# Performance work log

Hardware: AMD Instinct MI355X
Metric: run time of the kernel (lower is better)

The kernel has to match this reference:

```python
import jax, jax.numpy as jnp
import numpy as np

TAU = 2.0      # LIFNode default tau
V_TH = 1.0     # default v_threshold
ALPHA = 4.0    # surrogate.Sigmoid default alpha

@jax.custom_vjp
def spike_fn(x):
    # heaviside: spike if membrane potential crosses threshold
    return (x >= 0.0).astype(x.dtype)

def _spike_fwd(x):
    return spike_fn(x), x

def _spike_bwd(x, g):
    s = jax.nn.sigmoid(ALPHA * x)
    return (g * ALPHA * s * (1.0 - s),)

spike_fn.defvjp(_spike_fwd, _spike_bwd)

def lif_step(v, inp):
    # decay_input=True, v_reset=0.0 (hard reset):
    # v <- v + (inp - v)/tau ; spike = H(v - v_th) ; v <- v*(1-spike)
    v = v + (inp - v) / TAU
    s = spike_fn(v - V_TH)
    v = v * (1.0 - s)
    return v, s

def setup_inputs() -> dict:
    key = jax.random.key(0)
    k_x, k1, k2, k3 = jax.random.split(key, 4)
    T, B, H, W = 16, 64, 150, 400
    x = jax.random.normal(k_x, (T, B, H, W), dtype=jnp.float32)
    # torch Linear default init: U(-1/sqrt(fan_in), 1/sqrt(fan_in))
    def lin_init(k, out_f, in_f):
        bound = 1.0 / np.sqrt(in_f)
        return jax.random.uniform(k, (out_f, in_f), dtype=jnp.float32,
                                  minval=-bound, maxval=bound)
    W1 = lin_init(k1, 200, 60000)
    W2 = lin_init(k2, 50, 200)
    W3 = lin_init(k3, 2, 50)
    return {"x": x, "W1": W1, "W2": W2, "W3": W3}

def reference(x, W1, W2, W3):
    T, B = x.shape[0], x.shape[1]
    xf = x.reshape(T, B, -1)  # layer.Flatten over non-(T,B) dims -> [T,B,60000]
    D1, D2, D3 = W1.shape[0], W2.shape[0], W3.shape[0]

    def step(carry, xt):
        v1, v2, v3 = carry
        h1 = xt @ W1.T            # [B,200]
        v1, s1 = lif_step(v1, h1)
        h2 = s1 @ W2.T            # [B,50]
        v2, s2 = lif_step(v2, h2)
        h3 = s2 @ W3.T            # [B,2]
        v3, s3 = lif_step(v3, h3)
        return (v1, v2, v3), s3

    init = (jnp.zeros((B, D1), x.dtype),
            jnp.zeros((B, D2), x.dtype),
            jnp.zeros((B, D3), x.dtype))
    _, out = jax.lax.scan(step, init, xf)  # out: [T,B,2] spike trains
    return out
```

## Files before the change

kernel.cpp:

```cpp
#include <hip/hip_runtime.h>
#include <hip/hip_bf16.h>

#define T_STEPS 16
#define BATCH   64
#define M_ROWS  1024
#define K_DIM   60000
#define N1      200
#define N2      50
#define N3      2
#define HN      (M_ROWS * N1)
#define BK      32

typedef __attribute__((ext_vector_type(8)))  short bf16x8;
typedef __attribute__((ext_vector_type(16))) float f32x16;

static __device__ __forceinline__ bf16x8 cvt8(float4 lo, float4 hi) {
    union { bf16x8 v; __hip_bfloat162 h[4]; } u;
    u.h[0] = __float22bfloat162_rn(make_float2(lo.x, lo.y));
    u.h[1] = __float22bfloat162_rn(make_float2(lo.z, lo.w));
    u.h[2] = __float22bfloat162_rn(make_float2(hi.x, hi.y));
    u.h[3] = __float22bfloat162_rn(make_float2(hi.z, hi.w));
    return u.v;
}

static __device__ __forceinline__ float bf2f(unsigned short u) {
    unsigned int x = (unsigned int)u << 16;
    return __uint_as_float(x);
}

static __device__ __forceinline__ void lgkm_barrier() {
    __builtin_amdgcn_sched_barrier(0);
    asm volatile("s_waitcnt lgkmcnt(0)\n\ts_barrier" ::: "memory");
    __builtin_amdgcn_sched_barrier(0);
}

template <int KSEG, int KSTEPS, int NWG>
__global__ __launch_bounds__(512, 4)
void gemm_lds(const float* __restrict__ x,
              const float* __restrict__ w1,
              unsigned short* __restrict__ part) {
    __shared__ __align__(16) char smem[2][24576];

    const int tid = threadIdx.x;
    const int l   = tid & 63;
    const int wv  = tid >> 6;
    const int wm  = wv & 1;
    const int wn  = wv >> 1;

    const int hw      = blockIdx.y * 8 + blockIdx.x;
    const int logical = (hw & 7) * (NWG / 8) + (hw >> 3);
    const int s  = logical >> 3;
    const int mt = logical & 7;

    const int m0 = mt * 128;
    const int k0 = s * KSEG;

    const int ar = tid >> 2;
    const int ag = tid & 3;
    const float* asrc = x + (size_t)(m0 + ar) * K_DIM + k0 + ag * 8;
    const int aw_off = ar * 64 + ((ag ^ ((ar >> 1) & 3)) << 4);

    const int br = tid >> 1;
    const int bh = tid & 1;
    const bool bvalid = br < N1;
    const float* bsrc = w1 + (size_t)br * K_DIM + k0 + bh * 16;
    const int bg0 = bh * 2;
    const int bw_off0 = 8192 + br * 64 + (((bg0)     ^ ((br >> 1) & 3)) << 4);
    const int bw_off1 = 8192 + br * 64 + (((bg0 + 1) ^ ((br >> 1) & 3)) << 4);

    f32x16 acc[2][2];
    #pragma unroll
    for (int i = 0; i < 2; ++i)
        #pragma unroll
        for (int j = 0; j < 2; ++j)
            #pragma unroll
            for (int q = 0; q < 16; ++q) acc[i][j][q] = 0.f;

    float4 pA[2][2];
    float4 pB[4];

    {
        float4 a0 = *(const float4*)asrc;
        float4 a1 = *(const float4*)(asrc + 4);
        float4 b0, b1, b2, b3;
        if (bvalid) {
            b0 = *(const float4*)bsrc;
            b1 = *(const float4*)(bsrc + 4);
            b2 = *(const float4*)(bsrc + 8);
            b3 = *(const float4*)(bsrc + 12);
        }
        pA[1][0] = *(const float4*)(asrc + BK);
        pA[1][1] = *(const float4*)(asrc + BK + 4);
        if (bvalid) {
            const float* bp = bsrc + BK;
            pB[0] = *(const float4*)bp;
            pB[1] = *(const float4*)(bp + 4);
            pB[2] = *(const float4*)(bp + 8);
            pB[3] = *(const float4*)(bp + 12);
        }
        *(bf16x8*)(smem[0] + aw_off) = cvt8(a0, a1);
        if (bvalid) {
            *(bf16x8*)(smem[0] + bw_off0) = cvt8(b0, b1);
            *(bf16x8*)(smem[0] + bw_off1) = cvt8(b2, b3);
        }
    }
    lgkm_barrier();

    const int fr = l & 31;
    const int fh = (l >> 5) * 16;

    #pragma unroll
    for (int it = 0; it < KSTEPS; ++it) {
        const int cur = it & 1;
        const bool more = (it + 1) < KSTEPS;

        if (more) {
            const int jn = (it + 2 < KSTEPS) ? (it + 2) : (KSTEPS - 1);
            pA[cur][0] = *(const float4*)(asrc + jn * BK);
            pA[cur][1] = *(const float4*)(asrc + jn * BK + 4);
        }

        const char* ab = smem[cur];
        const char* bb = smem[cur] + 8192;
        #pragma unroll
        for (int kk = 0; kk < 2; ++kk) {
            const int r0 = wm * 64 + fr;
            const int r1 = wm * 64 + 32 + fr;
            bf16x8 a0 = *(const bf16x8*)(ab + r0 * 64 + ((kk * 32 + fh) ^ (((r0 >> 1) & 3) << 4)));
            bf16x8 a1 = *(const bf16x8*)(ab + r1 * 64 + ((kk * 32 + fh) ^ (((r1 >> 1) & 3) << 4)));
            #pragma unroll
            for (int fn = 0; fn < 2; ++fn) {
                if (wn == 3 && fn == 1) continue;
                const int n = wn * 64 + fn * 32 + fr;
                bf16x8 bv = *(const bf16x8*)(bb + n * 64 + ((kk * 32 + fh) ^ (((n >> 1) & 3) << 4)));
                acc[0][fn] = __builtin_amdgcn_mfma_f32_32x32x16_bf16(a0, bv, acc[0][fn], 0, 0, 0);
                acc[1][fn] = __builtin_amdgcn_mfma_f32_32x32x16_bf16(a1, bv, acc[1][fn], 0, 0, 0);
            }
        }

        if (more) {
            char* nb = smem[cur ^ 1];
            *(bf16x8*)(nb + aw_off) = cvt8(pA[cur ^ 1][0], pA[cur ^ 1][1]);
            if (bvalid) {
                *(bf16x8*)(nb + bw_off0) = cvt8(pB[0], pB[1]);
                *(bf16x8*)(nb + bw_off1) = cvt8(pB[2], pB[3]);
                if ((it + 2) < KSTEPS) {
                    const float* bp = bsrc + (size_t)(it + 2) * BK;
                    pB[0] = *(const float4*)bp;
                    pB[1] = *(const float4*)(bp + 4);
                    pB[2] = *(const float4*)(bp + 8);
                    pB[3] = *(const float4*)(bp + 12);
                }
            }
            lgkm_barrier();
        }
    }

    const int col = l & 31;
    const int rhi = (l >> 5) * 4;
    #pragma unroll
    for (int fm = 0; fm < 2; ++fm)
        #pragma unroll
        for (int fn = 0; fn < 2; ++fn) {
            const int gn = wn * 64 + fn * 32 + col;
            if (gn < N1) {
                const int gmb = m0 + wm * 64 + fm * 32 + rhi;
                #pragma unroll
                for (int r = 0; r < 16; ++r) {
                    const int gm = gmb + (r & 3) + 8 * (r >> 2);
                    __hip_bfloat16 hv = __float2bfloat16(acc[fm][fn][r]);
                    part[(size_t)s * HN + (size_t)gm * N1 + gn] = *(unsigned short*)&hv;
                }
            }
        }
}

template <int KSPLIT>
__global__ __launch_bounds__(256)
void reduce_kernel(const unsigned short* __restrict__ part, float* __restrict__ h1) {
    const size_t f = ((size_t)blockIdx.x * 256 + threadIdx.x) * 2;
    float a0 = 0.f, a1 = 0.f;
    #pragma unroll 25
    for (int s = 0; s < KSPLIT; ++s) {
        const unsigned int v = *(const unsigned int*)(part + (size_t)s * HN + f);
        a0 += bf2f((unsigned short)(v & 0xFFFFu));
        a1 += bf2f((unsigned short)(v >> 16));
    }
    h1[f]     = a0;
    h1[f + 1] = a1;
}

__global__ __launch_bounds__(256)
void tail_kernel(const float* __restrict__ h1,
                 const float* __restrict__ w2, const float* __restrict__ w3,
                 float* __restrict__ out) {
    __shared__ float w2s[N2 * N1];
    __shared__ float w3s[N3 * N2];
    __shared__ unsigned long long msk[T_STEPS][4];

    const int b    = blockIdx.x;
    const int i    = threadIdx.x;
    const int wv   = i >> 6;
    const int lane = i & 63;

    for (int o = i; o < (N2 * N1) / 4; o += 256)
        ((float4*)w2s)[o] = ((const float4*)w2)[o];
    if (i < N3 * N2) w3s[i] = w3[i];

    float h[T_STEPS];
    #pragma unroll
    for (int t = 0; t < T_STEPS; ++t)
        h[t] = (i < N1) ? h1[(size_t)(t * BATCH + b) * N1 + i] : 0.f;

    float v1 = 0.f;
    #pragma unroll
    for (int t = 0; t < T_STEPS; ++t) {
        v1 += (h[t] - v1) * 0.5f;
        bool sp = (v1 - 1.0f) >= 0.f;
        unsigned long long m = __ballot(sp);
        if (sp) v1 = 0.f;
        if (lane == 0) msk[t][wv] = m;
    }
    __syncthreads();

    if (wv == 0) {
        float v2 = 0.f, v3 = 0.f;
        for (int t = 0; t < T_STEPS; ++t) {
            float h2 = 0.f;
            if (lane < N2) {
                #pragma unroll
                for (int w = 0; w < 4; ++w) {
                    unsigned long long m = msk[t][w];
                    while (m) {
                        int lz = __builtin_ctzll(m);
                        m &= m - 1;
                        h2 += w2s[lane * N1 + (w * 64 + lz)];
                    }
                }
            }
            v2 += (h2 - v2) * 0.5f;
            bool sp2 = (v2 - 1.0f) >= 0.f;
            unsigned long long bal2 = __ballot(sp2);
            if (sp2) v2 = 0.f;

            float h3 = 0.f;
            if (lane < N3) {
                unsigned long long m = bal2;
                while (m) {
                    int j = __builtin_ctzll(m);
                    m &= m - 1;
                    h3 += w3s[lane * N2 + j];
                }
            }
            v3 += (h3 - v3) * 0.5f;
            bool sp3 = (v3 - 1.0f) >= 0.f;
            if (lane < N3)
                out[(size_t)(t * BATCH + b) * N3 + lane] = sp3 ? 1.f : 0.f;
            if (sp3) v3 = 0.f;
        }
    }
}

extern "C" void kernel_launch(void* const* d_in, const int* in_sizes, int n_in,
                              void* d_out, int out_size, void* d_ws, size_t ws_size,
                              hipStream_t stream) {
    const float* x  = (const float*)d_in[0];
    const float* w1 = (const float*)d_in[1];
    const float* w2 = (const float*)d_in[2];
    const float* w3 = (const float*)d_in[3];
    float* out = (float*)d_out;

    const size_t h1_bytes  = (size_t)HN * 4;
    const size_t need125 = (size_t)125 * HN * 2 + h1_bytes;
    const bool big = ws_size >= need125;

    const int ksplit = big ? 125 : 25;
    unsigned short* part = (unsigned short*)d_ws;
    float* h1 = (float*)((char*)d_ws + (size_t)ksplit * HN * 2);

    if (big) {
        dim3 g(8, 125);
        gemm_lds<480, 15, 1000><<<g, 512, 0, stream>>>(x, w1, part);
        reduce_kernel<125><<<HN / 512, 256, 0, stream>>>(part, h1);
    } else {
        dim3 g(8, 25);
        gemm_lds<2400, 75, 200><<<g, 512, 0, stream>>>(x, w1, part);
        reduce_kernel<25><<<HN / 512, 256, 0, stream>>>(part, h1);
    }
    tail_kernel<<<BATCH, 256, 0, stream>>>(h1, w2, w3, out);
}
```

Measured before the change: 99.06 us.

## Stage A tile with 64-wide K chunks per thread, refilled every other step

```diff
diff --git a/kernel.cpp b/kernel.cpp
--- a/kernel.cpp
+++ b/kernel.cpp
@@ -39,7 +39,8 @@
 void gemm_lds(const float* __restrict__ x,
               const float* __restrict__ w1,
               unsigned short* __restrict__ part) {
-    __shared__ __align__(16) char smem[2][24576];
+    __shared__ __align__(16) char smemA[2][16384];
+    __shared__ __align__(16) char smemB[2][16384];
 
     const int tid = threadIdx.x;
     const int l   = tid & 63;
@@ -55,33 +56,28 @@
     const int m0 = mt * 128;
     const int k0 = s * KSEG;
 
-    const int ar = tid >> 2;
-    const int ag = tid & 3;
-    const float* asrc = x + (size_t)(m0 + ar) * K_DIM + k0 + ag * 8;
-    const int aw_off = ar * 64 + ((ag ^ ((ar >> 1) & 3)) << 4);
+    const int ar  = tid >> 2;
+    const int ag2 = tid & 3;
+    const float* asrc = x + (size_t)(m0 + ar) * K_DIM + k0 + ag2 * 16;
+    const int awG0 = ar * 128 + (((2 * ag2)     ^ (ar & 7)) << 4);
+    const int awG1 = ar * 128 + (((2 * ag2 + 1) ^ (ar & 7)) << 4);
 
     const int br = tid >> 1;
     const int bh = tid & 1;
     const bool bvalid = br < N1;
     const float* bsrc = w1 + (size_t)br * K_DIM + k0 + bh * 16;
     const int bg0 = bh * 2;
-    const int bw_off0 = 8192 + br * 64 + (((bg0)     ^ ((br >> 1) & 3)) << 4);
-    const int bw_off1 = 8192 + br * 64 + (((bg0 + 1) ^ ((br >> 1) & 3)) << 4);
-
-    f32x16 acc[2][2];
-    #pragma unroll
-    for (int i = 0; i < 2; ++i)
-        #pragma unroll
-        for (int j = 0; j < 2; ++j)
-            #pragma unroll
-            for (int q = 0; q < 16; ++q) acc[i][j][q] = 0.f;
-
-    float4 pA[2][2];
+    const int bw_off0 = br * 64 + (((bg0)     ^ ((br >> 1) & 3)) << 4);
+    const int bw_off1 = br * 64 + (((bg0 + 1) ^ ((br >> 1) & 3)) << 4);
+
+    float4 pA[4];
     float4 pB[4];
 
     {
         float4 a0 = *(const float4*)asrc;
         float4 a1 = *(const float4*)(asrc + 4);
+        float4 a2 = *(const float4*)(asrc + 8);
+        float4 a3 = *(const float4*)(asrc + 12);
         float4 b0, b1, b2, b3;
         if (bvalid) {
             b0 = *(const float4*)bsrc;
@@ -89,67 +85,83 @@
             b2 = *(const float4*)(bsrc + 8);
             b3 = *(const float4*)(bsrc + 12);
         }
-        pA[1][0] = *(const float4*)(asrc + BK);
-        pA[1][1] = *(const float4*)(asrc + BK + 4);
+        pA[0] = *(const float4*)(asrc + 2 * BK);
+        pA[1] = *(const float4*)(asrc + 2 * BK + 4);
+        pA[2] = *(const float4*)(asrc + 2 * BK + 8);
+        pA[3] = *(const float4*)(asrc + 2 * BK + 12);
         if (bvalid) {
-            const float* bp = bsrc + BK;
-            pB[0] = *(const float4*)bp;
-            pB[1] = *(const float4*)(bp + 4);
-            pB[2] = *(const float4*)(bp + 8);
-            pB[3] = *(const float4*)(bp + 12);
-        }
-        *(bf16x8*)(smem[0] + aw_off) = cvt8(a0, a1);
+            pB[0] = *(const float4*)(bsrc + BK);
+            pB[1] = *(const float4*)(bsrc + BK + 4);
+            pB[2] = *(const float4*)(bsrc + BK + 8);
+            pB[3] = *(const float4*)(bsrc + BK + 12);
+        }
+        *(bf16x8*)(smemA[0] + awG0) = cvt8(a0, a1);
+        *(bf16x8*)(smemA[0] + awG1) = cvt8(a2, a3);
         if (bvalid) {
-            *(bf16x8*)(smem[0] + bw_off0) = cvt8(b0, b1);
-            *(bf16x8*)(smem[0] + bw_off1) = cvt8(b2, b3);
+            *(bf16x8*)(smemB[0] + bw_off0) = cvt8(b0, b1);
+            *(bf16x8*)(smemB[0] + bw_off1) = cvt8(b2, b3);
         }
     }
     lgkm_barrier();
 
+    f32x16 acc[2][2];
+    #pragma unroll
+    for (int i = 0; i < 2; ++i)
+        #pragma unroll
+        for (int j = 0; j < 2; ++j)
+            #pragma unroll
+            for (int q = 0; q < 16; ++q) acc[i][j][q] = 0.f;
+
     const int fr = l & 31;
-    const int fh = (l >> 5) * 16;
+    const int lh = l >> 5;
 
     #pragma unroll
     for (int it = 0; it < KSTEPS; ++it) {
-        const int cur = it & 1;
         const bool more = (it + 1) < KSTEPS;
 
-        if (more) {
-            const int jn = (it + 2 < KSTEPS) ? (it + 2) : (KSTEPS - 1);
-            pA[cur][0] = *(const float4*)(asrc + jn * BK);
-            pA[cur][1] = *(const float4*)(asrc + jn * BK + 4);
-        }
-
-        const char* ab = smem[cur];
-        const char* bb = smem[cur] + 8192;
+        const char* ab = smemA[(it >> 1) & 1];
+        const char* bb = smemB[it & 1];
         #pragma unroll
         for (int kk = 0; kk < 2; ++kk) {
             const int r0 = wm * 64 + fr;
             const int r1 = wm * 64 + 32 + fr;
-            bf16x8 a0 = *(const bf16x8*)(ab + r0 * 64 + ((kk * 32 + fh) ^ (((r0 >> 1) & 3) << 4)));
-            bf16x8 a1 = *(const bf16x8*)(ab + r1 * 64 + ((kk * 32 + fh) ^ (((r1 >> 1) & 3) << 4)));
+            const int GA = (it & 1) * 4 + kk * 2 + lh;
+            bf16x8 a0 = *(const bf16x8*)(ab + r0 * 128 + ((GA ^ (r0 & 7)) << 4));
+            bf16x8 a1 = *(const bf16x8*)(ab + r1 * 128 + ((GA ^ (r1 & 7)) << 4));
             #pragma unroll
             for (int fn = 0; fn < 2; ++fn) {
                 if (wn == 3 && fn == 1) continue;
                 const int n = wn * 64 + fn * 32 + fr;
-                bf16x8 bv = *(const bf16x8*)(bb + n * 64 + ((kk * 32 + fh) ^ (((n >> 1) & 3) << 4)));
+                bf16x8 bv = *(const bf16x8*)(bb + n * 64 + ((kk * 32 + lh * 16) ^ (((n >> 1) & 3) << 4)));
                 acc[0][fn] = __builtin_amdgcn_mfma_f32_32x32x16_bf16(a0, bv, acc[0][fn], 0, 0, 0);
                 acc[1][fn] = __builtin_amdgcn_mfma_f32_32x32x16_bf16(a1, bv, acc[1][fn], 0, 0, 0);
             }
         }
 
         if (more) {
-            char* nb = smem[cur ^ 1];
-            *(bf16x8*)(nb + aw_off) = cvt8(pA[cur ^ 1][0], pA[cur ^ 1][1]);
+            char* nbB = smemB[(it + 1) & 1];
             if (bvalid) {
-                *(bf16x8*)(nb + bw_off0) = cvt8(pB[0], pB[1]);
-                *(bf16x8*)(nb + bw_off1) = cvt8(pB[2], pB[3]);
+                *(bf16x8*)(nbB + bw_off0) = cvt8(pB[0], pB[1]);
+                *(bf16x8*)(nbB + bw_off1) = cvt8(pB[2], pB[3]);
                 if ((it + 2) < KSTEPS) {
                     const float* bp = bsrc + (size_t)(it + 2) * BK;
                     pB[0] = *(const float4*)bp;
                     pB[1] = *(const float4*)(bp + 4);
                     pB[2] = *(const float4*)(bp + 8);
                     pB[3] = *(const float4*)(bp + 12);
+                }
+            }
+            if (it & 1) {
+                char* nbA = smemA[((it + 1) >> 1) & 1];
+                *(bf16x8*)(nbA + awG0) = cvt8(pA[0], pA[1]);
+                *(bf16x8*)(nbA + awG1) = cvt8(pA[2], pA[3]);
+                const int base = (it + 3) * BK;
+                if (base + ag2 * 16 + 16 <= KSEG) {
+                    const float* ap = asrc + base;
+                    pA[0] = *(const float4*)ap;
+                    pA[1] = *(const float4*)(ap + 4);
+                    pA[2] = *(const float4*)(ap + 8);
+                    pA[3] = *(const float4*)(ap + 12);
                 }
             }
             lgkm_barrier();
```

Measured after the change: 103.1 us. 1.04x slower.

## Replace split-K partial buffer and reduce kernel with fp32 atomicAdd into h1

Applied to the files above, without the earlier changes.

```diff
diff --git a/kernel.cpp b/kernel.cpp
--- a/kernel.cpp
+++ b/kernel.cpp
@@ -23,22 +23,24 @@
     return u.v;
 }
 
-static __device__ __forceinline__ float bf2f(unsigned short u) {
-    unsigned int x = (unsigned int)u << 16;
-    return __uint_as_float(x);
-}
-
 static __device__ __forceinline__ void lgkm_barrier() {
     __builtin_amdgcn_sched_barrier(0);
     asm volatile("s_waitcnt lgkmcnt(0)\n\ts_barrier" ::: "memory");
     __builtin_amdgcn_sched_barrier(0);
 }
 
+__global__ __launch_bounds__(256)
+void zero_h1(float* __restrict__ h1) {
+    const size_t e = ((size_t)blockIdx.x * 256 + threadIdx.x) * 4;
+    if (e < (size_t)HN)
+        *(float4*)(h1 + e) = (float4){0.f, 0.f, 0.f, 0.f};
+}
+
 template <int KSEG, int KSTEPS, int NWG>
 __global__ __launch_bounds__(512, 4)
 void gemm_lds(const float* __restrict__ x,
               const float* __restrict__ w1,
-              unsigned short* __restrict__ part) {
+              float* __restrict__ h1) {
     __shared__ __align__(16) char smem[2][24576];
 
     const int tid = threadIdx.x;
@@ -168,26 +170,10 @@
                 #pragma unroll
                 for (int r = 0; r < 16; ++r) {
                     const int gm = gmb + (r & 3) + 8 * (r >> 2);
-                    __hip_bfloat16 hv = __float2bfloat16(acc[fm][fn][r]);
-                    part[(size_t)s * HN + (size_t)gm * N1 + gn] = *(unsigned short*)&hv;
-                }
-            }
-        }
-}
-
-template <int KSPLIT>
-__global__ __launch_bounds__(256)
-void reduce_kernel(const unsigned short* __restrict__ part, float* __restrict__ h1) {
-    const size_t f = ((size_t)blockIdx.x * 256 + threadIdx.x) * 2;
-    float a0 = 0.f, a1 = 0.f;
-    #pragma unroll 25
-    for (int s = 0; s < KSPLIT; ++s) {
-        const unsigned int v = *(const unsigned int*)(part + (size_t)s * HN + f);
-        a0 += bf2f((unsigned short)(v & 0xFFFFu));
-        a1 += bf2f((unsigned short)(v >> 16));
-    }
-    h1[f]     = a0;
-    h1[f + 1] = a1;
+                    atomicAdd(h1 + (size_t)gm * N1 + gn, acc[fm][fn][r]);
+                }
+            }
+        }
 }
 
 __global__ __launch_bounds__(256)
@@ -270,22 +256,10 @@
     const float* w3 = (const float*)d_in[3];
     float* out = (float*)d_out;
 
-    const size_t h1_bytes  = (size_t)HN * 4;
-    const size_t need125 = (size_t)125 * HN * 2 + h1_bytes;
-    const bool big = ws_size >= need125;
-
-    const int ksplit = big ? 125 : 25;
-    unsigned short* part = (unsigned short*)d_ws;
-    float* h1 = (float*)((char*)d_ws + (size_t)ksplit * HN * 2);
-
-    if (big) {
-        dim3 g(8, 125);
-        gemm_lds<480, 15, 1000><<<g, 512, 0, stream>>>(x, w1, part);
-        reduce_kernel<125><<<HN / 512, 256, 0, stream>>>(part, h1);
-    } else {
-        dim3 g(8, 25);
-        gemm_lds<2400, 75, 200><<<g, 512, 0, stream>>>(x, w1, part);
-        reduce_kernel<25><<<HN / 512, 256, 0, stream>>>(part, h1);
-    }
+    float* h1 = (float*)d_ws;
+
+    zero_h1<<<HN / (256 * 4), 256, 0, stream>>>(h1);
+    dim3 g(8, 125);
+    gemm_lds<480, 15, 1000><<<g, 512, 0, stream>>>(x, w1, h1);
     tail_kernel<<<BATCH, 256, 0, stream>>>(h1, w2, w3, out);
 }
```

Result: slower. 160.1 us (+61.6%).
